# Optimization experiments

Measured on AMD Instinct MI355X. Metric: run time of the kernel, lower is better.

Reference implementation:

```python
import jax, jax.numpy as jnp
import numpy as np

GROUP = 64       # quantization block size along in_features
SCALING = 2.0    # delta_alpha / r = 32 / 16


def setup_inputs() -> dict:
    key = jax.random.key(0)
    k1, k2, k3, k4 = jax.random.split(key, 4)
    B, S, D_IN, D_OUT = 8, 2048, 4096, 4096
    x = jax.random.normal(k1, (B, S, D_IN), dtype=jnp.float32)
    # int4 codes in [0, 16); symmetric zero-point 8
    w_codes = jax.random.randint(k2, (D_OUT, D_IN), 0, 16, dtype=jnp.int32)
    # per-(row, group) scales; small positive values like bnb absmax/7
    scales = jax.random.uniform(k3, (D_OUT, D_IN // GROUP), dtype=jnp.float32) * 0.02
    base_bias = jax.random.normal(k4, (D_OUT,), dtype=jnp.float32)
    delta_w = jax.random.normal(jax.random.fold_in(key, 5), (D_OUT, D_IN), dtype=jnp.float32) * 0.01
    return {"x": x, "w_codes": w_codes, "scales": scales,
            "base_bias": base_bias, "delta_w": delta_w}


def _dequant(w_codes, scales):
    # symmetric int4 dequant: w = (code - 8) * scale_of_its_group
    d_out, d_in = w_codes.shape
    w = (w_codes.astype(scales.dtype) - 8.0).reshape(d_out, d_in // GROUP, GROUP)
    w = w * scales[:, :, None]
    return w.reshape(d_out, d_in)


def reference(x, w_codes, scales, base_bias, delta_w):
    # base layer: int4 dequant-matmul + bias
    w = _dequant(w_codes, scales)                       # [D_out, D_in]
    base = jnp.einsum("bsi,oi->bso", x, w) + base_bias  # [B, S, D_out]
    # delta branch: dropout(p=0) -> matmul -> scale -> residual add
    delta = jnp.einsum("bsi,oi->bso", x, delta_w) * SCALING
    return base + delta
```

## Files before the change

### kernel.cpp

```cpp
#include <hip/hip_runtime.h>
#include <cstdint>

#define D_IN   4096
#define D_OUT  4096
#define MTOT   16384
#define SCALING 2.0f

#define BM 256
#define BN 256
#define BK 64
#define KT (D_IN / BK)

#define XBLOCKS ((MTOT * D_IN) / (256 * 8))
#define WBLOCKS ((D_OUT * D_IN) / (256 * 8))

typedef float  f32x4  __attribute__((ext_vector_type(4)));
typedef __bf16 bf16x8 __attribute__((ext_vector_type(8)));
typedef unsigned short ushort8 __attribute__((ext_vector_type(8)));
typedef int    int4v  __attribute__((ext_vector_type(4)));
typedef float  float4v __attribute__((ext_vector_type(4)));

__device__ __forceinline__ unsigned short f2bf(float f) {
  union { float f; unsigned u; } v; v.f = f;
  unsigned r = v.u + 0x7FFF + ((v.u >> 16) & 1);
  return (unsigned short)(r >> 16);
}

#define ASYNC16(g, l)                                                        \
  __builtin_amdgcn_global_load_lds(                                          \
      (const __attribute__((address_space(1))) unsigned int*)(g),            \
      (__attribute__((address_space(3))) unsigned int*)(l), 16, 0, 0)

#define BAR    __builtin_amdgcn_s_barrier()
#define VMW(n) asm volatile("s_waitcnt vmcnt(" #n ")" ::: "memory")

__global__ __launch_bounds__(256) void prep_kernel(const float* __restrict__ x,
                                                   unsigned short* __restrict__ xbf,
                                                   const int* __restrict__ codes,
                                                   const float* __restrict__ scales,
                                                   const float* __restrict__ delta,
                                                   unsigned short* __restrict__ weff) {
  const int bid = blockIdx.x;
  if (bid < XBLOCKS) {
    int i = (bid * 256 + threadIdx.x) * 8;
    float4v lo = *(const float4v*)(x + i);
    float4v hi = *(const float4v*)(x + i + 4);
    ushort8 o;
    o[0] = f2bf(lo[0]); o[1] = f2bf(lo[1]); o[2] = f2bf(lo[2]); o[3] = f2bf(lo[3]);
    o[4] = f2bf(hi[0]); o[5] = f2bf(hi[1]); o[6] = f2bf(hi[2]); o[7] = f2bf(hi[3]);
    *(ushort8*)(xbf + i) = o;
  } else {
    int i = ((bid - XBLOCKS) * 256 + threadIdx.x) * 8;
    int row = i >> 12;
    int col = i & (D_IN - 1);
    float s = scales[(row << 6) + (col >> 6)];
    int4v   c0 = *(const int4v*)(codes + i);
    int4v   c1 = *(const int4v*)(codes + i + 4);
    float4v d0 = *(const float4v*)(delta + i);
    float4v d1 = *(const float4v*)(delta + i + 4);
    ushort8 o;
    o[0] = f2bf((float)(c0[0] - 8) * s + SCALING * d0[0]);
    o[1] = f2bf((float)(c0[1] - 8) * s + SCALING * d0[1]);
    o[2] = f2bf((float)(c0[2] - 8) * s + SCALING * d0[2]);
    o[3] = f2bf((float)(c0[3] - 8) * s + SCALING * d0[3]);
    o[4] = f2bf((float)(c1[0] - 8) * s + SCALING * d1[0]);
    o[5] = f2bf((float)(c1[1] - 8) * s + SCALING * d1[1]);
    o[6] = f2bf((float)(c1[2] - 8) * s + SCALING * d1[2]);
    o[7] = f2bf((float)(c1[3] - 8) * s + SCALING * d1[3]);
    *(ushort8*)(weff + i) = o;
  }
}


#define STAGE_A(buf_, kt_, h_) do {                                          \
    char* d_ = &lds[buf_][h_][0] + tid * 16;                                 \
    const unsigned short* s_ = gA + (size_t)(h_) * 128 * D_IN + (kt_) * 64;  \
    ASYNC16(s_, d_);                                                         \
    ASYNC16(s_ + 64 * D_IN, d_ + 8192);                                      \
  } while (0)

#define STAGE_B(buf_, kt_, h_) do {                                          \
    char* d_ = &lds[buf_][2 + (h_)][0] + tid * 16;                           \
    const unsigned short* s_ = gB + (size_t)(h_) * 128 * D_IN + (kt_) * 64;  \
    ASYNC16(s_, d_);                                                         \
    ASYNC16(s_ + 64 * D_IN, d_ + 8192);                                      \
  } while (0)

#define RD_A(buf_, h_) do {                                                  \
    _Pragma("unroll")                                                        \
    for (int m2 = 0; m2 < 4; ++m2) {                                         \
      const char* p_ = &lds[buf_][wr][0] + ((h_)*4 + m2) * 2048 + rowb;      \
      A[m2][0] = *(const bf16x8*)(p_ + koff0);                               \
      A[m2][1] = *(const bf16x8*)(p_ + koff1);                               \
    } } while (0)

#define RD_B(buf_, h_, dst_) do {                                            \
    _Pragma("unroll")                                                        \
    for (int n2 = 0; n2 < 2; ++n2) {                                         \
      const char* p_ = &lds[buf_][2 + (wc >> 1)][0] + (wc & 1) * 8192 +      \
                       (h_) * 4096 + n2 * 2048 + rowb;                       \
      dst_[n2][0] = *(const bf16x8*)(p_ + koff0);                            \
      dst_[n2][1] = *(const bf16x8*)(p_ + koff1);                            \
    } } while (0)

#define MM16(bfr_, mh_, nh_) do {                                            \
    __builtin_amdgcn_s_setprio(1);                                           \
    _Pragma("unroll")                                                        \
    for (int m2 = 0; m2 < 4; ++m2) {                                         \
      _Pragma("unroll")                                                      \
      for (int n2 = 0; n2 < 2; ++n2) {                                       \
        acc[(mh_)*4 + m2][(nh_)*2 + n2] = __builtin_amdgcn_mfma_f32_16x16x32_bf16( \
            A[m2][0], bfr_[n2][0], acc[(mh_)*4 + m2][(nh_)*2 + n2], 0, 0, 0);      \
        acc[(mh_)*4 + m2][(nh_)*2 + n2] = __builtin_amdgcn_mfma_f32_16x16x32_bf16( \
            A[m2][1], bfr_[n2][1], acc[(mh_)*4 + m2][(nh_)*2 + n2], 0, 0, 0);      \
      } }                                                                    \
    __builtin_amdgcn_s_setprio(0);                                           \
  } while (0)

#define KTILE(buf_, g_, SA_, SB_, VM_) do {                                  \
                                                                     \
    if (SA_) STAGE_A((buf_) ^ 1, (g_) + 1, 0);                               \
    BAR;                                                                     \
    RD_A(buf_, 0);                                                           \
    RD_B(buf_, 0, B0);                                                       \
    MM16(B0, 0, 0);                                                          \
                                                                     \
    if (SA_) STAGE_A((buf_) ^ 1, (g_) + 1, 1);                               \
    BAR;                                                                     \
    RD_B(buf_, 1, B1);                                                       \
    MM16(B1, 0, 1);                                                          \
                                                                     \
    if (SB_) STAGE_B(buf_, (g_) + 2, 0);                                     \
    BAR;                                                                     \
    RD_A(buf_, 1);                                                           \
    MM16(B0, 1, 0);                                                          \
                                                                     \
    if (SB_) STAGE_B(buf_, (g_) + 2, 1);                                     \
    BAR;                                                                     \
    MM16(B1, 1, 1);                                                          \
    VM_;                                                                     \
  } while (0)

__global__ __launch_bounds__(512, 2) void gemm8_kernel(const unsigned short* __restrict__ xbf,
                                                       const unsigned short* __restrict__ weff,
                                                       const float* __restrict__ bias,
                                                       float* __restrict__ out) {
  __shared__ __attribute__((aligned(1024))) char lds[2][4][16384];

  const int tid  = threadIdx.x;
  const int lane = tid & 63;
  const int wid  = tid >> 6;
  const int wr   = wid >> 2;
  const int wc   = wid & 3;

  const int id  = blockIdx.x;
  const int nid = (id & 7) * 128 + (id >> 3);
  const int tn  = nid & 15;
  const int tm  = nid >> 4;

  const int rowb  = (lane & 15) * 128;
  const int kx    = (lane & 7) << 4;
  const int koff0 = (((lane >> 4) * 16) ^ kx);
  const int koff1 = ((64 + (lane >> 4) * 16) ^ kx);

  const int sr = tid >> 3;
  const int ke = ((tid & 7) ^ (sr & 7)) * 8;
  const unsigned short* gA = xbf  + (size_t)(tm * BM + sr) * D_IN + ke;
  const unsigned short* gB = weff + (size_t)(tn * BN + sr) * D_IN + ke;

  f32x4 acc[8][4] = {};
  bf16x8 A[4][2], B0[2][2], B1[2][2];

  STAGE_A(0, 0, 0); STAGE_A(0, 0, 1);
  STAGE_B(0, 0, 0); STAGE_B(0, 0, 1);
  STAGE_B(1, 1, 0); STAGE_B(1, 1, 1);
  VMW(4);

  for (int g = 0; g < KT - 2; g += 2) {
    KTILE(0, g,     1, 1, VMW(4));
    KTILE(1, g + 1, 1, 1, VMW(4));
  }
  KTILE(0, KT - 2, 1, 0, VMW(0));
  KTILE(1, KT - 1, 0, 0, (void)0);

  const int row0 = tm * BM + wr * 128 + (lane >> 4) * 4;
  const int col0 = tn * BN + wc * 64 + (lane & 15);
#pragma unroll
  for (int n = 0; n < 4; ++n) {
    const int col = col0 + n * 16;
    const float bv = bias[col];
#pragma unroll
    for (int m = 0; m < 8; ++m) {
      const int r = row0 + m * 16;
#pragma unroll
      for (int j = 0; j < 4; ++j)
        out[(size_t)(r + j) * D_OUT + col] = acc[m][n][j] + bv;
    }
  }
}

extern "C" void kernel_launch(void* const* d_in, const int* in_sizes, int n_in,
                              void* d_out, int out_size, void* d_ws, size_t ws_size,
                              hipStream_t stream) {
  const float* x      = (const float*)d_in[0];
  const int*   codes  = (const int*)d_in[1];
  const float* scales = (const float*)d_in[2];
  const float* bias   = (const float*)d_in[3];
  const float* delta  = (const float*)d_in[4];
  float* out = (float*)d_out;

  unsigned short* xbf  = (unsigned short*)d_ws;
  unsigned short* weff = xbf + (size_t)MTOT * D_IN;

  prep_kernel<<<XBLOCKS + WBLOCKS, 256, 0, stream>>>(x, xbf, codes, scales, delta, weff);

  gemm8_kernel<<<(MTOT / BM) * (D_OUT / BN), 512, 0, stream>>>(xbf, weff, bias, out);
}
```

Measured before the change: 554.5 us.

## Shrink GEMM tile to 256x128x32 with 4 waves and a new staging pipeline

```diff
diff --git a/kernel.cpp b/kernel.cpp
--- a/kernel.cpp
+++ b/kernel.cpp
@@ -7,8 +7,8 @@
 #define SCALING 2.0f
 
 #define BM 256
-#define BN 256
-#define BK 64
+#define BN 128
+#define BK 32
 #define KT (D_IN / BK)
 
 #define XBLOCKS ((MTOT * D_IN) / (256 * 8))
@@ -72,116 +72,107 @@
 }
 
 
-#define STAGE_A(buf_, kt_, h_) do {                                          \
-    char* d_ = &lds[buf_][h_][0] + tid * 16;                                 \
-    const unsigned short* s_ = gA + (size_t)(h_) * 128 * D_IN + (kt_) * 64;  \
+#define STAGE_A01(buf_, kt_) do {                                            \
+    char* d_ = &lds[buf_][0] + tid * 16;                                     \
+    const unsigned short* s_ = gA + (size_t)(kt_) * 32;                      \
     ASYNC16(s_, d_);                                                         \
-    ASYNC16(s_ + 64 * D_IN, d_ + 8192);                                      \
-  } while (0)
-
-#define STAGE_B(buf_, kt_, h_) do {                                          \
-    char* d_ = &lds[buf_][2 + (h_)][0] + tid * 16;                           \
-    const unsigned short* s_ = gB + (size_t)(h_) * 128 * D_IN + (kt_) * 64;  \
+    ASYNC16(s_ + 32 * D_IN, d_ + 4096);                                      \
+  } while (0)
+
+#define STAGE_A23(buf_, kt_) do {                                            \
+    char* d_ = &lds[buf_][0] + tid * 16 + 8192;                              \
+    const unsigned short* s_ = gA + (size_t)(kt_) * 32 + 64 * D_IN;          \
     ASYNC16(s_, d_);                                                         \
-    ASYNC16(s_ + 64 * D_IN, d_ + 8192);                                      \
-  } while (0)
-
-#define RD_A(buf_, h_) do {                                                  \
+    ASYNC16(s_ + 32 * D_IN, d_ + 4096);                                      \
+  } while (0)
+
+#define STAGE_B01(buf_, kt_) do {                                            \
+    char* d_ = &lds[buf_][0] + tid * 16 + 16384;                             \
+    const unsigned short* s_ = gB + (size_t)(kt_) * 32;                      \
+    ASYNC16(s_, d_);                                                         \
+    ASYNC16(s_ + 32 * D_IN, d_ + 4096);                                      \
+  } while (0)
+
+#define RD_A(buf_, mh_) do {                                                 \
     _Pragma("unroll")                                                        \
     for (int m2 = 0; m2 < 4; ++m2) {                                         \
-      const char* p_ = &lds[buf_][wr][0] + ((h_)*4 + m2) * 2048 + rowb;      \
-      A[m2][0] = *(const bf16x8*)(p_ + koff0);                               \
-      A[m2][1] = *(const bf16x8*)(p_ + koff1);                               \
+      const char* p_ = &lds[buf_][0] + ((mh_)*4 + m2) * 2048 + rowb + koffA; \
+      A[m2] = *(const bf16x8*)p_;                                            \
     } } while (0)
 
-#define RD_B(buf_, h_, dst_) do {                                            \
+#define RD_B(buf_) do {                                                      \
     _Pragma("unroll")                                                        \
-    for (int n2 = 0; n2 < 2; ++n2) {                                         \
-      const char* p_ = &lds[buf_][2 + (wc >> 1)][0] + (wc & 1) * 8192 +      \
-                       (h_) * 4096 + n2 * 2048 + rowb;                       \
-      dst_[n2][0] = *(const bf16x8*)(p_ + koff0);                            \
-      dst_[n2][1] = *(const bf16x8*)(p_ + koff1);                            \
+    for (int n2 = 0; n2 < 4; ++n2) {                                         \
+      const char* p_ = &lds[buf_][0] + 16384 + n2 * 2048 + rowb + koffB;     \
+      Bf[n2] = *(const bf16x8*)p_;                                           \
     } } while (0)
 
-#define MM16(bfr_, mh_, nh_) do {                                            \
+#define MM16(mh_) do {                                                       \
     __builtin_amdgcn_s_setprio(1);                                           \
     _Pragma("unroll")                                                        \
     for (int m2 = 0; m2 < 4; ++m2) {                                         \
       _Pragma("unroll")                                                      \
-      for (int n2 = 0; n2 < 2; ++n2) {                                       \
-        acc[(mh_)*4 + m2][(nh_)*2 + n2] = __builtin_amdgcn_mfma_f32_16x16x32_bf16( \
-            A[m2][0], bfr_[n2][0], acc[(mh_)*4 + m2][(nh_)*2 + n2], 0, 0, 0);      \
-        acc[(mh_)*4 + m2][(nh_)*2 + n2] = __builtin_amdgcn_mfma_f32_16x16x32_bf16( \
-            A[m2][1], bfr_[n2][1], acc[(mh_)*4 + m2][(nh_)*2 + n2], 0, 0, 0);      \
+      for (int n2 = 0; n2 < 4; ++n2) {                                       \
+        acc[(mh_)*4 + m2][n2] = __builtin_amdgcn_mfma_f32_16x16x32_bf16(     \
+            A[m2], Bf[n2], acc[(mh_)*4 + m2][n2], 0, 0, 0);                  \
       } }                                                                    \
     __builtin_amdgcn_s_setprio(0);                                           \
   } while (0)
 
-#define KTILE(buf_, g_, SA_, SB_, VM_) do {                                  \
+#define KTILE(buf_, g_, S_, VM0_, VM1_) do {                                 \
                                                                      \
-    if (SA_) STAGE_A((buf_) ^ 1, (g_) + 1, 0);                               \
+    if (S_) { STAGE_A01((buf_) ^ 1, (g_) + 1); STAGE_B01((buf_) ^ 1, (g_) + 1); } \
+    VM0_;                                                                    \
     BAR;                                                                     \
     RD_A(buf_, 0);                                                           \
-    RD_B(buf_, 0, B0);                                                       \
-    MM16(B0, 0, 0);                                                          \
+    RD_B(buf_);                                                              \
+    MM16(0);                                                                 \
                                                                      \
-    if (SA_) STAGE_A((buf_) ^ 1, (g_) + 1, 1);                               \
-    BAR;                                                                     \
-    RD_B(buf_, 1, B1);                                                       \
-    MM16(B1, 0, 1);                                                          \
-                                                                     \
-    if (SB_) STAGE_B(buf_, (g_) + 2, 0);                                     \
+    if (S_) STAGE_A23((buf_) ^ 1, (g_) + 1);                                 \
+    VM1_;                                                                    \
     BAR;                                                                     \
     RD_A(buf_, 1);                                                           \
-    MM16(B0, 1, 0);                                                          \
-                                                                     \
-    if (SB_) STAGE_B(buf_, (g_) + 2, 1);                                     \
-    BAR;                                                                     \
-    MM16(B1, 1, 1);                                                          \
-    VM_;                                                                     \
-  } while (0)
-
-__global__ __launch_bounds__(512, 2) void gemm8_kernel(const unsigned short* __restrict__ xbf,
+    MM16(1);                                                                 \
+  } while (0)
+
+__global__ __launch_bounds__(256, 2) void gemm4_kernel(const unsigned short* __restrict__ xbf,
                                                        const unsigned short* __restrict__ weff,
                                                        const float* __restrict__ bias,
                                                        float* __restrict__ out) {
-  __shared__ __attribute__((aligned(1024))) char lds[2][4][16384];
+  __shared__ __attribute__((aligned(1024))) char lds[2][24576];
 
   const int tid  = threadIdx.x;
   const int lane = tid & 63;
   const int wid  = tid >> 6;
-  const int wr   = wid >> 2;
-  const int wc   = wid & 3;
+  const int wr   = wid >> 1;
+  const int wc   = wid & 1;
 
   const int id  = blockIdx.x;
-  const int nid = (id & 7) * 128 + (id >> 3);
-  const int tn  = nid & 15;
-  const int tm  = nid >> 4;
+  const int nid = (id & 7) * 256 + (id >> 3);
+  const int tn  = nid & 31;
+  const int tm  = nid >> 5;
 
   const int rowb  = (lane & 15) * 128;
-  const int kx    = (lane & 7) << 4;
-  const int koff0 = (((lane >> 4) * 16) ^ kx);
-  const int koff1 = ((64 + (lane >> 4) * 16) ^ kx);
-
-  const int sr = tid >> 3;
-  const int ke = ((tid & 7) ^ (sr & 7)) * 8;
-  const unsigned short* gA = xbf  + (size_t)(tm * BM + sr) * D_IN + ke;
-  const unsigned short* gB = weff + (size_t)(tn * BN + sr) * D_IN + ke;
+  const int koffA = ((((lane >> 4) | (wr << 2))) ^ (lane & 7)) << 4;
+  const int koffB = ((((lane >> 4) | (wc << 2))) ^ (lane & 7)) << 4;
+
+  const int cc = (tid & 7) ^ ((tid >> 3) & 7);
+  const unsigned short* gA = xbf  + (size_t)(tm * BM + (tid >> 3) + 128 * (cc >> 2)) * D_IN + (cc & 3) * 8;
+  const unsigned short* gB = weff + (size_t)(tn * BN + (tid >> 3) +  64 * (cc >> 2)) * D_IN + (cc & 3) * 8;
 
   f32x4 acc[8][4] = {};
-  bf16x8 A[4][2], B0[2][2], B1[2][2];
-
-  STAGE_A(0, 0, 0); STAGE_A(0, 0, 1);
-  STAGE_B(0, 0, 0); STAGE_B(0, 0, 1);
-  STAGE_B(1, 1, 0); STAGE_B(1, 1, 1);
-  VMW(4);
+  bf16x8 A[4], Bf[4];
+
+  STAGE_A01(0, 0);
+  STAGE_B01(0, 0);
+  STAGE_A23(0, 0);
 
   for (int g = 0; g < KT - 2; g += 2) {
-    KTILE(0, g,     1, 1, VMW(4));
-    KTILE(1, g + 1, 1, 1, VMW(4));
+    KTILE(0, g,     1, VMW(6), VMW(6));
+    KTILE(1, g + 1, 1, VMW(6), VMW(6));
   }
-  KTILE(0, KT - 2, 1, 0, VMW(0));
-  KTILE(1, KT - 1, 0, 0, (void)0);
+  KTILE(0, KT - 2, 1, VMW(6), VMW(6));
+  KTILE(1, KT - 1, 0, VMW(2), VMW(0));
 
   const int row0 = tm * BM + wr * 128 + (lane >> 4) * 4;
   const int col0 = tn * BN + wc * 64 + (lane & 15);
@@ -214,5 +205,5 @@
 
   prep_kernel<<<XBLOCKS + WBLOCKS, 256, 0, stream>>>(x, xbf, codes, scales, delta, weff);
 
-  gemm8_kernel<<<(MTOT / BM) * (D_OUT / BN), 512, 0, stream>>>(xbf, weff, bias, out);
-}
+  gemm4_kernel<<<(MTOT / BM) * (D_OUT / BN), 256, 0, stream>>>(xbf, weff, bias, out);
+}
```

Result: slower. 751.9 us (+35.6%).
